# Kernel optimization log

Measured on AMD Instinct MI355X. Metric: run time of the kernel, lower is better.

## Reference

```python
import jax, jax.numpy as jnp
import numpy as np

H = 181  # hidden size

def setup_inputs() -> dict:
    key = jax.random.key(0)
    ks = jax.random.split(key, 7)
    B, T, I, C = 1024, 1024, 1, 10
    x = jax.random.normal(ks[0], (B, T, I), dtype=jnp.float32)
    w_ih = jax.random.normal(ks[1], (3 * H, I), dtype=jnp.float32) * 0.5
    w_hh = jax.random.normal(ks[2], (3 * H, H), dtype=jnp.float32) * (1.0 / np.sqrt(H))
    b_ih = jax.random.normal(ks[3], (3 * H,), dtype=jnp.float32) * 0.1
    b_hh = jax.random.normal(ks[4], (3 * H,), dtype=jnp.float32) * 0.1
    w_fc = jax.random.normal(ks[5], (C, H), dtype=jnp.float32) * (1.0 / np.sqrt(H))
    b_fc = jax.random.normal(ks[6], (C,), dtype=jnp.float32) * 0.1
    return {"x": x, "w_ih": w_ih, "w_hh": w_hh, "b_ih": b_ih, "b_hh": b_hh,
            "w_fc": w_fc, "b_fc": b_fc}

def _gru_last_hidden(x, w_ih, w_hh, b_ih, b_hh):
    # x: [B, T, I]. Precompute input-side gate pre-activations for all steps.
    B = x.shape[0]
    gi = jnp.einsum('bti,gi->btg', x, w_ih) + b_ih  # [B, T, 3H]
    gi = jnp.swapaxes(gi, 0, 1)                     # [T, B, 3H] for scan
    h0 = jnp.zeros((B, H), dtype=x.dtype)

    def step(h, gi_t):
        gh = h @ w_hh.T + b_hh                      # [B, 3H]
        r = jax.nn.sigmoid(gi_t[:, :H] + gh[:, :H])
        z = jax.nn.sigmoid(gi_t[:, H:2 * H] + gh[:, H:2 * H])
        n = jnp.tanh(gi_t[:, 2 * H:] + r * gh[:, 2 * H:])
        h_new = (1.0 - z) * n + z * h
        return h_new, None

    h_last, _ = jax.lax.scan(step, h0, gi)
    return h_last  # [B, H]

def reference(x, w_ih, w_hh, b_ih, b_hh, w_fc, b_fc):
    h_last = _gru_last_hidden(x, w_ih, w_hh, b_ih, b_hh)
    logits = h_last @ w_fc.T + b_fc  # [B, num_classes]
    return logits
```

## Files before the change

### kernel.cpp

```cpp
#include <hip/hip_runtime.h>

#define H 181
#define T_LEN 1024
#define BB 4
#define NBLK 256
#define NTHR 768
#define FRAGB 1024
#define PST 192
#define XSTR 1027

typedef __attribute__((ext_vector_type(4))) int intx4;

#define LOG2E 1.4426950408889634f
#define SCH_C  1064992506.0f
#define SCH_LO 897220352.0f
#define SCH_HI 1182433024.0f

__device__ __forceinline__ float exp2_fast(float g) {
    float s = fmaf(g, 8388608.0f, SCH_C);
    s = fminf(fmaxf(s, SCH_LO), SCH_HI);
    return __uint_as_float((unsigned)s);
}
__device__ __forceinline__ float rcpf(float x)   { return __builtin_amdgcn_rcpf(x); }
__device__ __forceinline__ float exp2hw(float x) { return __builtin_amdgcn_exp2f(x); }

__device__ __forceinline__ float rowscale(const float* wrow, bool mv) {
    float rm = 0.0f;
    if (mv)
        for (int k = 0; k < H; ++k) rm = fmaxf(rm, fabsf(wrow[k]));
    return (rm > 1e-30f) ? rm * (1.0f / 127.0f) : 1.0f;
}
__device__ __forceinline__ intx4 build_frag(const float* wrow, float invs,
                                            int kbase, bool mv) {
    intx4 f;
    #pragma unroll
    for (int w = 0; w < 4; ++w) {
        int dw = 0;
        #pragma unroll
        for (int e = 0; e < 4; ++e) {
            int k = kbase + w * 4 + e;
            float v = (mv && k < H) ? wrow[k] * invs : 0.0f;
            v = fminf(fmaxf(rintf(v), -127.0f), 127.0f);
            dw |= (((int)v) & 255) << (8 * e);
        }
        f[w] = dw;
    }
    return f;
}

#define MFMA8(A, B, C) __builtin_amdgcn_mfma_i32_16x16x64_i8((A), (B), (C), 0, 0, 0)

__launch_bounds__(NTHR, 3)
__global__ void gru_i8(const float* __restrict__ x,
                       const float* __restrict__ w_ih,
                       const float* __restrict__ w_hh,
                       const float* __restrict__ b_ih,
                       const float* __restrict__ b_hh,
                       const float* __restrict__ w_fc,
                       const float* __restrict__ b_fc,
                       float* __restrict__ out) {
    __shared__ __align__(16) char  hfr_s[2 * 3 * FRAGB];
    __shared__ __align__(16) float x_s[BB * XSTR];
    __shared__ float wsc_s[3 * PST];
    __shared__ volatile char pad_s[57344];

    const int tid  = threadIdx.x;
    const int jt   = tid >> 6;
    const int lane = tid & 63;
    const int col  = lane & 15;
    const int q    = lane >> 4;
    const int b0   = blockIdx.x * BB;
    if (tid == 0) pad_s[0] = 0;

    const int  mu = jt * 16 + col;
    const bool mv = (mu < H);
    const float* wrow0 = w_hh + (size_t)(0 * H + (mv ? mu : 0)) * H;
    const float* wrow1 = w_hh + (size_t)(1 * H + (mv ? mu : 0)) * H;
    const float* wrow2 = w_hh + (size_t)(2 * H + (mv ? mu : 0)) * H;
    const float sc0 = rowscale(wrow0, mv);
    const float sc1 = rowscale(wrow1, mv);
    const float sc2 = rowscale(wrow2, mv);
    const float iv0 = 1.0f / sc0, iv1 = 1.0f / sc1, iv2 = 1.0f / sc2;
    const int   kb  = q * 16;
    const intx4 aR0 = build_frag(wrow0, iv0, kb,       mv);
    const intx4 aR1 = build_frag(wrow0, iv0, kb +  64, mv);
    const intx4 aR2 = build_frag(wrow0, iv0, kb + 128, mv);
    const intx4 aZ0 = build_frag(wrow1, iv1, kb,       mv);
    const intx4 aZ1 = build_frag(wrow1, iv1, kb +  64, mv);
    const intx4 aZ2 = build_frag(wrow1, iv1, kb + 128, mv);
    const intx4 aN0 = build_frag(wrow2, iv2, kb,       mv);
    const intx4 aN1 = build_frag(wrow2, iv2, kb +  64, mv);
    const intx4 aN2 = build_frag(wrow2, iv2, kb + 128, mv);
    if (q == 0) {
        wsc_s[0 * PST + mu] = sc0;
        wsc_s[1 * PST + mu] = sc1;
        wsc_s[2 * PST + mu] = sc2;
    }

    for (int i = tid; i < BB * T_LEN; i += NTHR) {
        int bb = i >> 10, t = i & 1023;
        x_s[bb * XSTR + t] = x[(size_t)b0 * T_LEN + i];
    }
    {
        int* hz = (int*)hfr_s;
        for (int i = tid; i < 2 * 3 * FRAGB / 4; i += NTHR) hz[i] = 0;
    }
    __syncthreads();

    const int  rr4 = (col >> 2) & 3;
    const int  b   = col & 3;
    const int  u   = jt * 16 + q * 4 + rr4;
    const bool jv  = (u < H);
    const float dqR = -LOG2E * wsc_s[0 * PST + u] * (1.0f / 127.0f);
    const float dqZ = -LOG2E * wsc_s[1 * PST + u] * (1.0f / 127.0f);
    const float dqN =  2.0f * LOG2E * wsc_s[2 * PST + u] * (1.0f / 127.0f);
    const float baseR = jv ? -LOG2E * (b_ih[u] + b_hh[u])             : 0.0f;
    const float baseZ = jv ? -LOG2E * (b_ih[H + u] + b_hh[H + u])     : 0.0f;
    const float baseN = jv ?  2.0f * LOG2E * b_hh[2 * H + u]          : 0.0f;
    const float wrS = jv ? -LOG2E * w_ih[u]                : 0.0f;
    const float wzS = jv ? -LOG2E * w_ih[H + u]            : 0.0f;
    const float wnS = jv ?  2.0f * LOG2E * w_ih[2 * H + u] : 0.0f;
    const float bnI = jv ?  2.0f * LOG2E * b_ih[2 * H + u] : 0.0f;
    const int woffB = (jt >> 2) * FRAGB + (((jt & 3) * 16 + b) * 16) + q * 4;
    const int rbase = lane * 16;

    float h = 0.0f;

    char* rb = hfr_s;
    char* wb = hfr_s + 3 * FRAGB;

    for (int t = 0; t < T_LEN; ++t) {
        const intx4 bf0 = *(const intx4*)(rb + 0 * FRAGB + rbase);
        const intx4 bf1 = *(const intx4*)(rb + 1 * FRAGB + rbase);
        const intx4 bf2 = *(const intx4*)(rb + 2 * FRAGB + rbase);

        intx4 cR = {0, 0, 0, 0}, cZ = {0, 0, 0, 0}, cN = {0, 0, 0, 0};
        cR = MFMA8(aR0, bf0, cR); cR = MFMA8(aR1, bf1, cR); cR = MFMA8(aR2, bf2, cR);
        cZ = MFMA8(aZ0, bf0, cZ); cZ = MFMA8(aZ1, bf1, cZ); cZ = MFMA8(aZ2, bf2, cZ);
        cN = MFMA8(aN0, bf0, cN); cN = MFMA8(aN1, bf1, cN); cN = MFMA8(aN2, bf2, cN);

        int vR = cR[0], vZ = cZ[0], vN = cN[0];
        vR = __builtin_amdgcn_update_dpp(vR, cR[1], 0x114, 0xF, 0x2, false);
        vR = __builtin_amdgcn_update_dpp(vR, cR[2], 0x118, 0xF, 0x4, false);
        vR = __builtin_amdgcn_update_dpp(vR, cR[3], 0x11C, 0xF, 0x8, false);
        vZ = __builtin_amdgcn_update_dpp(vZ, cZ[1], 0x114, 0xF, 0x2, false);
        vZ = __builtin_amdgcn_update_dpp(vZ, cZ[2], 0x118, 0xF, 0x4, false);
        vZ = __builtin_amdgcn_update_dpp(vZ, cZ[3], 0x11C, 0xF, 0x8, false);
        vN = __builtin_amdgcn_update_dpp(vN, cN[1], 0x114, 0xF, 0x2, false);
        vN = __builtin_amdgcn_update_dpp(vN, cN[2], 0x118, 0xF, 0x4, false);
        vN = __builtin_amdgcn_update_dpp(vN, cN[3], 0x11C, 0xF, 0x8, false);

        float pR = fmaf((float)vR, dqR, baseR);
        float pZ = fmaf((float)vZ, dqZ, baseZ);
        float pN = fmaf((float)vN, dqN, baseN);
        float xv = x_s[b * XSTR + t];

        float er = exp2_fast(fmaf(xv, wrS, pR));
        float ez = exp2hw(fminf(fmaf(xv, wzS, pZ), 14.0f));
        float dR = 1.0f + er, dZ = 1.0f + ez;
        float qq = rcpf(dR * dZ);
        float rr = qq * dZ, zz = qq * dR;
        float gn = fmaf(rr, pN, fmaf(xv, wnS, bnI));
        float en = exp2hw(fminf(gn, 30.0f));
        float nn = fmaf(-2.0f, rcpf(1.0f + en), 1.0f);
        h = fmaf(zz, h - nn, nn);

        int iq = (int)rintf(h * 127.0f);
        int hq = jv ? (iq & 255) : 0;
        int t1 = __builtin_amdgcn_update_dpp(0, hq, 0x104, 0xF, 0xF, true);
        int t2 = __builtin_amdgcn_update_dpp(0, hq, 0x108, 0xF, 0xF, true);
        int t3 = __builtin_amdgcn_update_dpp(0, hq, 0x10C, 0xF, 0xF, true);
        int p01 = __builtin_amdgcn_perm(t1, hq, 0x05010400);
        int p23 = __builtin_amdgcn_perm(t3, t2, 0x05010400);
        int pk  = __builtin_amdgcn_perm(p23, p01, 0x05040100);
        if (rr4 == 0)
            *(int*)(wb + woffB) = pk;
        __syncthreads();

        char* tmp = rb; rb = wb; wb = tmp;
    }

    __syncthreads();
    x_s[b * PST + u] = h;
    __syncthreads();
    if (tid < BB * 10) {
        int bb = tid / 10, c = tid % 10;
        float acc = b_fc[c];
        for (int k = 0; k < H; ++k)
            acc = fmaf(x_s[bb * PST + k], w_fc[c * H + k], acc);
        out[(b0 + bb) * 10 + c] = acc;
    }
}

extern "C" void kernel_launch(void* const* d_in, const int* in_sizes, int n_in,
                              void* d_out, int out_size, void* d_ws, size_t ws_size,
                              hipStream_t stream) {
    const float* x    = (const float*)d_in[0];
    const float* w_ih = (const float*)d_in[1];
    const float* w_hh = (const float*)d_in[2];
    const float* b_ih = (const float*)d_in[3];
    const float* b_hh = (const float*)d_in[4];
    const float* w_fc = (const float*)d_in[5];
    const float* b_fc = (const float*)d_in[6];
    float* out = (float*)d_out;

    gru_i8<<<NBLK, NTHR, 0, stream>>>(x, w_ih, w_hh, b_ih, b_hh, w_fc, b_fc, out);
}
```

Baseline: 754.9 us.

## Halve batch per block and give each wave two output tiles

Each block now handles 2 batch rows with 6 waves, and each wave computes two 16-row tiles of the hidden units. Twice as many blocks are launched. The DPP packing is reworked so a single lane set holds results for both tiles and both batch entries, which raises MFMA utilization per lane in the elementwise gate math. The shared-memory padding that capped occupancy is removed. In exchange, each wave holds twice the weight fragments in registers and runs more serialized MFMA work per step, and MFMA columns are still mostly wasted on padding since only 2 of 16 batch columns carry data.

```diff
diff --git a/kernel.cpp b/kernel.cpp
--- a/kernel.cpp
+++ b/kernel.cpp
@@ -2,9 +2,9 @@
 
 #define H 181
 #define T_LEN 1024
-#define BB 4
-#define NBLK 256
-#define NTHR 768
+#define BB 2
+#define NBLK 512
+#define NTHR 384
 #define FRAGB 1024
 #define PST 192
 #define XSTR 1027
@@ -49,6 +49,8 @@
 }
 
 #define MFMA8(A, B, C) __builtin_amdgcn_mfma_i32_16x16x64_i8((A), (B), (C), 0, 0, 0)
+#define DPP(OLD, SRC, CTL, BM) \
+    __builtin_amdgcn_update_dpp((OLD), (SRC), (CTL), 0xF, (BM), false)
 
 __launch_bounds__(NTHR, 3)
 __global__ void gru_i8(const float* __restrict__ x,
@@ -62,7 +64,6 @@
     __shared__ __align__(16) char  hfr_s[2 * 3 * FRAGB];
     __shared__ __align__(16) float x_s[BB * XSTR];
     __shared__ float wsc_s[3 * PST];
-    __shared__ volatile char pad_s[57344];
 
     const int tid  = threadIdx.x;
     const int jt   = tid >> 6;
@@ -70,31 +71,42 @@
     const int col  = lane & 15;
     const int q    = lane >> 4;
     const int b0   = blockIdx.x * BB;
-    if (tid == 0) pad_s[0] = 0;
-
-    const int  mu = jt * 16 + col;
-    const bool mv = (mu < H);
-    const float* wrow0 = w_hh + (size_t)(0 * H + (mv ? mu : 0)) * H;
-    const float* wrow1 = w_hh + (size_t)(1 * H + (mv ? mu : 0)) * H;
-    const float* wrow2 = w_hh + (size_t)(2 * H + (mv ? mu : 0)) * H;
-    const float sc0 = rowscale(wrow0, mv);
-    const float sc1 = rowscale(wrow1, mv);
-    const float sc2 = rowscale(wrow2, mv);
-    const float iv0 = 1.0f / sc0, iv1 = 1.0f / sc1, iv2 = 1.0f / sc2;
-    const int   kb  = q * 16;
-    const intx4 aR0 = build_frag(wrow0, iv0, kb,       mv);
-    const intx4 aR1 = build_frag(wrow0, iv0, kb +  64, mv);
-    const intx4 aR2 = build_frag(wrow0, iv0, kb + 128, mv);
-    const intx4 aZ0 = build_frag(wrow1, iv1, kb,       mv);
-    const intx4 aZ1 = build_frag(wrow1, iv1, kb +  64, mv);
-    const intx4 aZ2 = build_frag(wrow1, iv1, kb + 128, mv);
-    const intx4 aN0 = build_frag(wrow2, iv2, kb,       mv);
-    const intx4 aN1 = build_frag(wrow2, iv2, kb +  64, mv);
-    const intx4 aN2 = build_frag(wrow2, iv2, kb + 128, mv);
+
+    const int  mu0 = (2 * jt + 0) * 16 + col;
+    const int  mu1 = (2 * jt + 1) * 16 + col;
+    const bool mv0 = (mu0 < H);
+    const bool mv1 = (mu1 < H);
+    const float* wR0 = w_hh + (size_t)(0 * H + (mv0 ? mu0 : 0)) * H;
+    const float* wZ0 = w_hh + (size_t)(1 * H + (mv0 ? mu0 : 0)) * H;
+    const float* wN0 = w_hh + (size_t)(2 * H + (mv0 ? mu0 : 0)) * H;
+    const float* wR1 = w_hh + (size_t)(0 * H + (mv1 ? mu1 : 0)) * H;
+    const float* wZ1 = w_hh + (size_t)(1 * H + (mv1 ? mu1 : 0)) * H;
+    const float* wN1 = w_hh + (size_t)(2 * H + (mv1 ? mu1 : 0)) * H;
+    const float scR0 = rowscale(wR0, mv0), scZ0 = rowscale(wZ0, mv0), scN0 = rowscale(wN0, mv0);
+    const float scR1 = rowscale(wR1, mv1), scZ1 = rowscale(wZ1, mv1), scN1 = rowscale(wN1, mv1);
+    const int kb = q * 16;
+    const intx4 fR00 = build_frag(wR0, 1.0f / scR0, kb,       mv0);
+    const intx4 fR01 = build_frag(wR0, 1.0f / scR0, kb +  64, mv0);
+    const intx4 fR02 = build_frag(wR0, 1.0f / scR0, kb + 128, mv0);
+    const intx4 fZ00 = build_frag(wZ0, 1.0f / scZ0, kb,       mv0);
+    const intx4 fZ01 = build_frag(wZ0, 1.0f / scZ0, kb +  64, mv0);
+    const intx4 fZ02 = build_frag(wZ0, 1.0f / scZ0, kb + 128, mv0);
+    const intx4 fN00 = build_frag(wN0, 1.0f / scN0, kb,       mv0);
+    const intx4 fN01 = build_frag(wN0, 1.0f / scN0, kb +  64, mv0);
+    const intx4 fN02 = build_frag(wN0, 1.0f / scN0, kb + 128, mv0);
+    const intx4 fR10 = build_frag(wR1, 1.0f / scR1, kb,       mv1);
+    const intx4 fR11 = build_frag(wR1, 1.0f / scR1, kb +  64, mv1);
+    const intx4 fR12 = build_frag(wR1, 1.0f / scR1, kb + 128, mv1);
+    const intx4 fZ10 = build_frag(wZ1, 1.0f / scZ1, kb,       mv1);
+    const intx4 fZ11 = build_frag(wZ1, 1.0f / scZ1, kb +  64, mv1);
+    const intx4 fZ12 = build_frag(wZ1, 1.0f / scZ1, kb + 128, mv1);
+    const intx4 fN10 = build_frag(wN1, 1.0f / scN1, kb,       mv1);
+    const intx4 fN11 = build_frag(wN1, 1.0f / scN1, kb +  64, mv1);
+    const intx4 fN12 = build_frag(wN1, 1.0f / scN1, kb + 128, mv1);
     if (q == 0) {
-        wsc_s[0 * PST + mu] = sc0;
-        wsc_s[1 * PST + mu] = sc1;
-        wsc_s[2 * PST + mu] = sc2;
+        wsc_s[0 * PST + mu0] = scR0;  wsc_s[0 * PST + mu1] = scR1;
+        wsc_s[1 * PST + mu0] = scZ0;  wsc_s[1 * PST + mu1] = scZ1;
+        wsc_s[2 * PST + mu0] = scN0;  wsc_s[2 * PST + mu1] = scN1;
     }
 
     for (int i = tid; i < BB * T_LEN; i += NTHR) {
@@ -107,9 +119,10 @@
     }
     __syncthreads();
 
-    const int  rr4 = (col >> 2) & 3;
-    const int  b   = col & 3;
-    const int  u   = jt * 16 + q * 4 + rr4;
+    const int  rr4 = (lane >> 2) & 3;
+    const int  tau = (lane >> 1) & 1;
+    const int  b   = lane & 1;
+    const int  u   = (2 * jt + tau) * 16 + q * 4 + rr4;
     const bool jv  = (u < H);
     const float dqR = -LOG2E * wsc_s[0 * PST + u] * (1.0f / 127.0f);
     const float dqZ = -LOG2E * wsc_s[1 * PST + u] * (1.0f / 127.0f);
@@ -121,7 +134,8 @@
     const float wzS = jv ? -LOG2E * w_ih[H + u]            : 0.0f;
     const float wnS = jv ?  2.0f * LOG2E * w_ih[2 * H + u] : 0.0f;
     const float bnI = jv ?  2.0f * LOG2E * b_ih[2 * H + u] : 0.0f;
-    const int woffB = (jt >> 2) * FRAGB + (((jt & 3) * 16 + b) * 16) + q * 4;
+    const int u0    = (2 * jt + tau) * 16 + q * 4;
+    const int woffB = (u0 >> 6) * FRAGB + (((u0 >> 4) & 3) * 16 + b) * 16 + (u0 & 15);
     const int rbase = lane * 16;
 
     float h = 0.0f;
@@ -134,21 +148,41 @@
         const intx4 bf1 = *(const intx4*)(rb + 1 * FRAGB + rbase);
         const intx4 bf2 = *(const intx4*)(rb + 2 * FRAGB + rbase);
 
-        intx4 cR = {0, 0, 0, 0}, cZ = {0, 0, 0, 0}, cN = {0, 0, 0, 0};
-        cR = MFMA8(aR0, bf0, cR); cR = MFMA8(aR1, bf1, cR); cR = MFMA8(aR2, bf2, cR);
-        cZ = MFMA8(aZ0, bf0, cZ); cZ = MFMA8(aZ1, bf1, cZ); cZ = MFMA8(aZ2, bf2, cZ);
-        cN = MFMA8(aN0, bf0, cN); cN = MFMA8(aN1, bf1, cN); cN = MFMA8(aN2, bf2, cN);
-
-        int vR = cR[0], vZ = cZ[0], vN = cN[0];
-        vR = __builtin_amdgcn_update_dpp(vR, cR[1], 0x114, 0xF, 0x2, false);
-        vR = __builtin_amdgcn_update_dpp(vR, cR[2], 0x118, 0xF, 0x4, false);
-        vR = __builtin_amdgcn_update_dpp(vR, cR[3], 0x11C, 0xF, 0x8, false);
-        vZ = __builtin_amdgcn_update_dpp(vZ, cZ[1], 0x114, 0xF, 0x2, false);
-        vZ = __builtin_amdgcn_update_dpp(vZ, cZ[2], 0x118, 0xF, 0x4, false);
-        vZ = __builtin_amdgcn_update_dpp(vZ, cZ[3], 0x11C, 0xF, 0x8, false);
-        vN = __builtin_amdgcn_update_dpp(vN, cN[1], 0x114, 0xF, 0x2, false);
-        vN = __builtin_amdgcn_update_dpp(vN, cN[2], 0x118, 0xF, 0x4, false);
-        vN = __builtin_amdgcn_update_dpp(vN, cN[3], 0x11C, 0xF, 0x8, false);
+        intx4 a0 = {0, 0, 0, 0}, a1 = {0, 0, 0, 0};
+        a0 = MFMA8(fR00, bf0, a0); a0 = MFMA8(fR01, bf1, a0); a0 = MFMA8(fR02, bf2, a0);
+        a1 = MFMA8(fR10, bf0, a1); a1 = MFMA8(fR11, bf1, a1); a1 = MFMA8(fR12, bf2, a1);
+        int vR = a0[0];
+        vR = DPP(vR, a0[1], 0x114, 0x2);
+        vR = DPP(vR, a0[2], 0x118, 0x4);
+        vR = DPP(vR, a0[3], 0x11C, 0x8);
+        vR = DPP(vR, a1[0], 0x112, 0x1);
+        vR = DPP(vR, a1[1], 0x116, 0x2);
+        vR = DPP(vR, a1[2], 0x11A, 0x4);
+        vR = DPP(vR, a1[3], 0x11E, 0x8);
+
+        a0 = (intx4){0, 0, 0, 0}; a1 = (intx4){0, 0, 0, 0};
+        a0 = MFMA8(fZ00, bf0, a0); a0 = MFMA8(fZ01, bf1, a0); a0 = MFMA8(fZ02, bf2, a0);
+        a1 = MFMA8(fZ10, bf0, a1); a1 = MFMA8(fZ11, bf1, a1); a1 = MFMA8(fZ12, bf2, a1);
+        int vZ = a0[0];
+        vZ = DPP(vZ, a0[1], 0x114, 0x2);
+        vZ = DPP(vZ, a0[2], 0x118, 0x4);
+        vZ = DPP(vZ, a0[3], 0x11C, 0x8);
+        vZ = DPP(vZ, a1[0], 0x112, 0x1);
+        vZ = DPP(vZ, a1[1], 0x116, 0x2);
+        vZ = DPP(vZ, a1[2], 0x11A, 0x4);
+        vZ = DPP(vZ, a1[3], 0x11E, 0x8);
+
+        a0 = (intx4){0, 0, 0, 0}; a1 = (intx4){0, 0, 0, 0};
+        a0 = MFMA8(fN00, bf0, a0); a0 = MFMA8(fN01, bf1, a0); a0 = MFMA8(fN02, bf2, a0);
+        a1 = MFMA8(fN10, bf0, a1); a1 = MFMA8(fN11, bf1, a1); a1 = MFMA8(fN12, bf2, a1);
+        int vN = a0[0];
+        vN = DPP(vN, a0[1], 0x114, 0x2);
+        vN = DPP(vN, a0[2], 0x118, 0x4);
+        vN = DPP(vN, a0[3], 0x11C, 0x8);
+        vN = DPP(vN, a1[0], 0x112, 0x1);
+        vN = DPP(vN, a1[1], 0x116, 0x2);
+        vN = DPP(vN, a1[2], 0x11A, 0x4);
+        vN = DPP(vN, a1[3], 0x11E, 0x8);
 
         float pR = fmaf((float)vR, dqR, baseR);
         float pZ = fmaf((float)vZ, dqZ, baseZ);
```

Measured after the change: 1.644 ms. +117.7%, slower.
